# Performance work log

Measured on AMD Instinct MI355X. Metric: run time of the kernel, lower is better.

## Reference

```python
import jax, jax.numpy as jnp
import numpy as np

E = 1024   # embed_dim
H = 16     # num_heads
Dh = E // H
FF = 4 * E
LN_EPS = 1e-5


def _layernorm(x, g, b):
    mu = jnp.mean(x, axis=-1, keepdims=True)
    var = jnp.var(x, axis=-1, keepdims=True)
    return (x - mu) * jax.lax.rsqrt(var + LN_EPS) * g + b


def setup_inputs() -> dict:
    key = jax.random.key(0)
    ks = jax.random.split(key, 10)
    s = lambda fan_in: 1.0 / np.sqrt(fan_in)
    x = jax.random.normal(ks[0], (2, 2048, E), dtype=jnp.float32)
    Wq = jax.random.uniform(ks[1], (H, E, Dh), jnp.float32, -s(E), s(E))
    Wk = jax.random.uniform(ks[2], (H, E, Dh), jnp.float32, -s(E), s(E))
    Wproj = jax.random.uniform(ks[3], (E, E), jnp.float32, -s(E), s(E))
    bproj = jax.random.uniform(ks[4], (E,), jnp.float32, -s(E), s(E))
    ln1_g = jnp.ones((E,), jnp.float32)
    ln1_b = jnp.zeros((E,), jnp.float32)
    ln2_g = jnp.ones((E,), jnp.float32)
    ln2_b = jnp.zeros((E,), jnp.float32)
    W1 = jax.random.uniform(ks[5], (E, FF), jnp.float32, -s(E), s(E))
    b1 = jax.random.uniform(ks[6], (FF,), jnp.float32, -s(E), s(E))
    W2 = jax.random.uniform(ks[7], (FF, E), jnp.float32, -s(FF), s(FF))
    b2 = jax.random.uniform(ks[8], (E,), jnp.float32, -s(FF), s(FF))
    return dict(x=x, Wq=Wq, Wk=Wk, Wproj=Wproj, bproj=bproj,
                ln1_g=ln1_g, ln1_b=ln1_b, ln2_g=ln2_g, ln2_b=ln2_b,
                W1=W1, b1=b1, W2=W2, b2=b2)


def reference(x, Wq, Wk, Wproj, bproj, ln1_g, ln1_b, ln2_g, ln2_b, W1, b1, W2, b2):
    B, S, _ = x.shape
    # --- self-attention branch ---
    h = _layernorm(x, ln1_g, ln1_b)
    Q = jnp.einsum('bse,hed->bhsd', h, Wq)
    K = jnp.einsum('bse,hed->bhsd', h, Wk)
    # NOTE: original code uses V = key(x), so values == keys (faithful bug).
    scores = jnp.einsum('bhqd,bhkd->bhqk', Q, K) * (1.0 / np.sqrt(Dh))
    causal = jnp.tril(jnp.ones((S, S), dtype=bool))
    scores = jnp.where(causal, scores, -jnp.inf)
    attn = jax.nn.softmax(scores, axis=-1)  # dropout is identity in eval
    out = jnp.einsum('bhqk,bhkd->bhqd', attn, K)
    out = out.transpose(0, 2, 1, 3).reshape(B, S, H * Dh)
    x = x + out @ Wproj + bproj
    # --- MLP branch ---
    h2 = _layernorm(x, ln2_g, ln2_b)
    ff = jax.nn.relu(h2 @ W1 + b1) @ W2 + b2
    return x + ff
```

## Files before the change

### kernel.cpp

```cpp
#include <hip/hip_runtime.h>
#include <stdint.h>

typedef __bf16 bf16x8 __attribute__((ext_vector_type(8)));
typedef float f32x4 __attribute__((ext_vector_type(4)));
typedef float f32x16 __attribute__((ext_vector_type(16)));
typedef unsigned short u16;
typedef unsigned int u32;
typedef unsigned int u32x2 __attribute__((ext_vector_type(2)));

__device__ __forceinline__ u16 f2bf(float f) {
    u32 u = __builtin_bit_cast(u32, f);
    u = (u + 0x7fffu + ((u >> 16) & 1u)) >> 16;
    return (u16)u;
}
__device__ __forceinline__ float bf2f(u16 x) {
    return __builtin_bit_cast(float, (u32)x << 16);
}
__device__ __forceinline__ float fexp2(float x) {
#if __has_builtin(__builtin_amdgcn_exp2f)
    return __builtin_amdgcn_exp2f(x);
#else
    return exp2f(x);
#endif
}
__device__ __forceinline__ void plswap(u32& a, u32& b) {
#if __has_builtin(__builtin_amdgcn_permlane32_swap)
    u32x2 r = __builtin_amdgcn_permlane32_swap(a, b, false, false);
    a = r[0]; b = r[1];
#else
    asm volatile("v_permlane32_swap_b32 %0, %1" : "+v"(a), "+v"(b));
#endif
}

__device__ __forceinline__ void gload16(const u16* g, u16* l) {
    __builtin_amdgcn_global_load_lds(
        (const __attribute__((address_space(1))) unsigned int*)g,
        (__attribute__((address_space(3))) unsigned int*)l,
        16, 0, 0);
}

__device__ __constant__ unsigned char QB2[72] = {
    0,1,2,2,3,3,4,4,4,5,5,5,6,6,6,6,7,7,7,7,
    8,8,8,8,8,9,9,9,9,9,10,10,10,10,10,10,11,11,11,11,11,11,
    12,12,12,12,12,12,12,13,13,13,13,13,13,13,
    14,14,14,14,14,14,14,14,15,15,15,15,15,15,15,15};
__device__ __constant__ unsigned char CH2[72] = {
    0,0,0,1,0,1,0,1,2,0,1,2,0,1,2,3,0,1,2,3,
    0,1,2,3,4,0,1,2,3,4,0,1,2,3,4,5,0,1,2,3,4,5,
    0,1,2,3,4,5,6,0,1,2,3,4,5,6,
    0,1,2,3,4,5,6,7,0,1,2,3,4,5,6,7};
__device__ __constant__ unsigned char CUM2[17] =
    {0,1,2,4,6,9,12,16,20,25,30,36,42,49,56,64,72};

__global__ __launch_bounds__(256)
void prep_all(const float* __restrict__ Wq, const float* __restrict__ Wk,
              const float* __restrict__ Wproj, const float* __restrict__ W1,
              const float* __restrict__ W2,
              u16* __restrict__ wqkT, u16* __restrict__ wprojT,
              u16* __restrict__ w1T, u16* __restrict__ w2T,
              const float* __restrict__ x, const float* __restrict__ g1,
              const float* __restrict__ b1v, u16* __restrict__ hbuf) {
    __shared__ u16 tile[64 * 64];
    __shared__ float red[8];
    const int bid = blockIdx.x;
    const int t = threadIdx.x;
    if (bid >= 2816) {
        const int row = bid - 2816;
        float4 v = reinterpret_cast<const float4*>(x + (size_t)row * 1024)[t];
        float s = v.x + v.y + v.z + v.w;
        float sq = v.x * v.x + v.y * v.y + v.z * v.z + v.w * v.w;
        for (int o = 32; o > 0; o >>= 1) { s += __shfl_down(s, o); sq += __shfl_down(sq, o); }
        if ((t & 63) == 0) { red[t >> 6] = s; red[4 + (t >> 6)] = sq; }
        __syncthreads();
        float S  = red[0] + red[1] + red[2] + red[3];
        float SQ = red[4] + red[5] + red[6] + red[7];
        float mean = S * (1.f / 1024.f);
        float var  = SQ * (1.f / 1024.f) - mean * mean;
        float rstd = rsqrtf(var + 1e-5f);
        float4 g4 = reinterpret_cast<const float4*>(g1)[t];
        float4 b4 = reinterpret_cast<const float4*>(b1v)[t];
        ushort4 o;
        o.x = f2bf((v.x - mean) * rstd * g4.x + b4.x);
        o.y = f2bf((v.y - mean) * rstd * g4.y + b4.y);
        o.z = f2bf((v.z - mean) * rstd * g4.z + b4.z);
        o.w = f2bf((v.w - mean) * rstd * g4.w + b4.w);
        reinterpret_cast<ushort4*>(hbuf + (size_t)row * 1024)[t] = o;
        return;
    }
    const float* src; u16* dst; int R, C, c0, r0; size_t zb = 0;
    if (bid < 512) {
        const int q = bid & 255; const int z = q >> 4;
        src = (bid < 256) ? Wq : Wk;
        dst = (bid < 256) ? wqkT : (wqkT + 1048576);
        R = 1024; C = 64; c0 = 0; r0 = (q & 15) * 64; zb = (size_t)z * 65536;
    } else if (bid < 768) {
        const int q = bid - 512; src = Wproj; dst = wprojT; R = 1024; C = 1024;
        c0 = (q & 15) * 64; r0 = (q >> 4) * 64;
    } else if (bid < 1792) {
        const int q = bid - 768; src = W1; dst = w1T; R = 1024; C = 4096;
        c0 = (q & 63) * 64; r0 = (q >> 6) * 64;
    } else {
        const int q = bid - 1792; src = W2; dst = w2T; R = 4096; C = 1024;
        c0 = (q & 15) * 64; r0 = (q >> 4) * 64;
    }
    {
        const int r = t >> 2, j4 = t & 3;
        #pragma unroll
        for (int j = 0; j < 4; ++j) {
            int c = j4 * 4 + j * 16;
            float4 v = *reinterpret_cast<const float4*>(src + zb + (size_t)(r0 + r) * C + c0 + c);
            tile[(c + 0) * 64 + (r ^ (((c + 0) & 7) * 8))] = f2bf(v.x);
            tile[(c + 1) * 64 + (r ^ (((c + 1) & 7) * 8))] = f2bf(v.y);
            tile[(c + 2) * 64 + (r ^ (((c + 2) & 7) * 8))] = f2bf(v.z);
            tile[(c + 3) * 64 + (r ^ (((c + 3) & 7) * 8))] = f2bf(v.w);
        }
    }
    __syncthreads();
    {
        const int cc = t >> 2, j4 = t & 3;
        const int sw = (cc & 7) * 8;
        #pragma unroll
        for (int j2 = 0; j2 < 4; ++j2) {
            int rbase = j4 * 16 + j2 * 4;
            ushort4 o;
            o.x = tile[cc * 64 + ((rbase + 0) ^ sw)];
            o.y = tile[cc * 64 + ((rbase + 1) ^ sw)];
            o.z = tile[cc * 64 + ((rbase + 2) ^ sw)];
            o.w = tile[cc * 64 + ((rbase + 3) ^ sw)];
            *reinterpret_cast<ushort4*>(dst + zb + (size_t)(c0 + cc) * R + r0 + rbase) = o;
        }
    }
}

__global__ __launch_bounds__(256)
void ln_kernel(const float* __restrict__ x, u16* __restrict__ out,
               const float* __restrict__ gw, const float* __restrict__ bw) {
    __shared__ float red[8];
    int row = blockIdx.x, t = threadIdx.x;
    float4 v = reinterpret_cast<const float4*>(x + (size_t)row * 1024)[t];
    float s = v.x + v.y + v.z + v.w;
    float sq = v.x * v.x + v.y * v.y + v.z * v.z + v.w * v.w;
    for (int o = 32; o > 0; o >>= 1) { s += __shfl_down(s, o); sq += __shfl_down(sq, o); }
    if ((t & 63) == 0) { red[t >> 6] = s; red[4 + (t >> 6)] = sq; }
    __syncthreads();
    float S  = red[0] + red[1] + red[2] + red[3];
    float SQ = red[4] + red[5] + red[6] + red[7];
    float mean = S * (1.f / 1024.f);
    float var  = SQ * (1.f / 1024.f) - mean * mean;
    float rstd = rsqrtf(var + 1e-5f);
    float4 g4 = reinterpret_cast<const float4*>(gw)[t];
    float4 b4 = reinterpret_cast<const float4*>(bw)[t];
    ushort4 o;
    o.x = f2bf((v.x - mean) * rstd * g4.x + b4.x);
    o.y = f2bf((v.y - mean) * rstd * g4.y + b4.y);
    o.z = f2bf((v.z - mean) * rstd * g4.z + b4.z);
    o.w = f2bf((v.w - mean) * rstd * g4.w + b4.w);
    reinterpret_cast<ushort4*>(out + (size_t)row * 1024)[t] = o;
}

__global__ __launch_bounds__(256)
void ln2red_kernel(const u16* __restrict__ p0, const u16* __restrict__ p1,
                   const float4* __restrict__ x4, const float* __restrict__ bproj,
                   const float* __restrict__ gw, const float* __restrict__ bw,
                   float4* __restrict__ xmid, u16* __restrict__ out) {
    __shared__ float red[8];
    const int row = blockIdx.x, t = threadIdx.x;
    const size_t idx = (size_t)row * 256 + t;
    const ushort4 a4 = *reinterpret_cast<const ushort4*>(p0 + idx * 4);
    const ushort4 b4u = *reinterpret_cast<const ushort4*>(p1 + idx * 4);
    float4 xx = x4[idx];
    const float4 bp = *reinterpret_cast<const float4*>(bproj + (t << 2));
    float4 v;
    v.x = bf2f(a4.x) + bf2f(b4u.x) + xx.x + bp.x;
    v.y = bf2f(a4.y) + bf2f(b4u.y) + xx.y + bp.y;
    v.z = bf2f(a4.z) + bf2f(b4u.z) + xx.z + bp.z;
    v.w = bf2f(a4.w) + bf2f(b4u.w) + xx.w + bp.w;
    xmid[idx] = v;
    float s = v.x + v.y + v.z + v.w;
    float sq = v.x * v.x + v.y * v.y + v.z * v.z + v.w * v.w;
    for (int o = 32; o > 0; o >>= 1) { s += __shfl_down(s, o); sq += __shfl_down(sq, o); }
    if ((t & 63) == 0) { red[t >> 6] = s; red[4 + (t >> 6)] = sq; }
    __syncthreads();
    float S  = red[0] + red[1] + red[2] + red[3];
    float SQ = red[4] + red[5] + red[6] + red[7];
    float mean = S * (1.f / 1024.f);
    float var  = SQ * (1.f / 1024.f) - mean * mean;
    float rstd = rsqrtf(var + 1e-5f);
    const float4 g4 = *reinterpret_cast<const float4*>(gw + (t << 2));
    const float4 b4 = *reinterpret_cast<const float4*>(bw + (t << 2));
    ushort4 o;
    o.x = f2bf((v.x - mean) * rstd * g4.x + b4.x);
    o.y = f2bf((v.y - mean) * rstd * g4.y + b4.y);
    o.z = f2bf((v.z - mean) * rstd * g4.z + b4.z);
    o.w = f2bf((v.w - mean) * rstd * g4.w + b4.w);
    *reinterpret_cast<ushort4*>(out + idx * 4) = o;
}

template<int EPI, typename OT>
__global__ __launch_bounds__(256)
void gemm_bt(const u16* __restrict__ A, const u16* __restrict__ B,
             OT* __restrict__ C, const float* __restrict__ bias,
             const float* __restrict__ res, int K, int N, u16* __restrict__ ktr) {
    __shared__ u16 Al[128 * 64];
    __shared__ u16 Bl[128 * 64];
    const int t = threadIdx.x;
    const int lane = t & 63;
    const int w = t >> 6;
    const int wm = w >> 1, wn = w & 1;
    const int l15 = lane & 15, gq = lane >> 4;
    const int gx = gridDim.x;
    const int nwg = gx * gridDim.y;
    const int bid = blockIdx.y * gx + blockIdx.x;
    const int sw = ((nwg & 7) == 0) ? ((bid & 7) * (nwg >> 3) + (bid >> 3)) : bid;
    const int col0 = (sw % gx) * 128;
    const int row0 = (sw / gx) * 128;

    f32x4 acc[4][4] = {};

    const int nkb = K >> 6;
    for (int kb = 0; kb < nkb; ++kb) {
        #pragma unroll
        for (int i = 0; i < 4; ++i) {
            int slot = i * 256 + t;
            int r = slot >> 3;
            int g = (slot & 7) ^ (r & 7);
            gload16(A + (size_t)(row0 + r) * K + kb * 64 + g * 8, Al + slot * 8);
            gload16(B + (size_t)(col0 + r) * K + kb * 64 + g * 8, Bl + slot * 8);
        }
        __syncthreads();
        #pragma unroll
        for (int s = 0; s < 2; ++s) {
            bf16x8 af[4], bfr[4];
            #pragma unroll
            for (int mi = 0; mi < 4; ++mi) {
                int rl = wm * 64 + mi * 16 + l15;
                int ba = rl * 128 + ((s * 64 + gq * 16) ^ ((rl & 7) << 4));
                af[mi] = *reinterpret_cast<const bf16x8*>(reinterpret_cast<const char*>(Al) + ba);
            }
            #pragma unroll
            for (int ni = 0; ni < 4; ++ni) {
                int rl = wn * 64 + ni * 16 + l15;
                int ba = rl * 128 + ((s * 64 + gq * 16) ^ ((rl & 7) << 4));
                bfr[ni] = *reinterpret_cast<const bf16x8*>(reinterpret_cast<const char*>(Bl) + ba);
            }
            #pragma unroll
            for (int mi = 0; mi < 4; ++mi)
                #pragma unroll
                for (int ni = 0; ni < 4; ++ni)
                    acc[mi][ni] = __builtin_amdgcn_mfma_f32_16x16x32_bf16(af[mi], bfr[ni], acc[mi][ni], 0, 0, 0);
        }
        __syncthreads();
    }

    #pragma unroll
    for (int mi = 0; mi < 4; ++mi) {
        #pragma unroll
        for (int ni = 0; ni < 4; ++ni) {
            int gcol = col0 + wn * 64 + ni * 16 + l15;
            int grow0 = row0 + wm * 64 + mi * 16 + gq * 4;
            #pragma unroll
            for (int r = 0; r < 4; ++r) {
                int grow = grow0 + r;
                float v = acc[mi][ni][r];
                if constexpr (EPI == 1 || EPI == 2) v += bias[gcol];
                if constexpr (EPI == 1) v += res[(size_t)grow * N + gcol];
                if constexpr (EPI == 2) v = fmaxf(v, 0.f);
                if constexpr (sizeof(OT) == 4) C[(size_t)grow * N + gcol] = v;
                else                           C[(size_t)grow * N + gcol] = f2bf(v);
            }
        }
    }
}

#define DS_A(MH) \
  _Pragma("unroll") \
  for (int mi = 0; mi < 4; ++mi) { \
    const int rl = wm * 128 + (MH) * 64 + mi * 16 + l15; \
    const char* rp = abase + rl * 128; \
    const int sw2 = (rl & 7) << 4; \
    af[mi][0] = *reinterpret_cast<const bf16x8*>(rp + ((gq * 16) ^ sw2)); \
    af[mi][1] = *reinterpret_cast<const bf16x8*>(rp + ((64 + gq * 16) ^ sw2)); \
  }

#define DS_B(NH) \
  _Pragma("unroll") \
  for (int ni = 0; ni < 2; ++ni) { \
    const int rl = wn * 64 + (NH) * 32 + ni * 16 + l15; \
    const char* rp = bbase + rl * 128; \
    const int sw2 = (rl & 7) << 4; \
    bfr[NH][ni][0] = *reinterpret_cast<const bf16x8*>(rp + ((gq * 16) ^ sw2)); \
    bfr[NH][ni][1] = *reinterpret_cast<const bf16x8*>(rp + ((64 + gq * 16) ^ sw2)); \
  }

#define ST_A(HALF, KP, DB) \
  _Pragma("unroll") \
  for (int i = 0; i < 2; ++i) { \
    const int idx = i * 512 + t; const int rs = idx >> 3; const int kc = idx & 7; \
    const int row = (rs & 63) + ((rs >> 6) << 7) + (HALF) * 64; \
    gload16(Ag + (size_t)(row0 + row) * Kf + (KP) + ((kc ^ (row & 7)) << 3), (DB) + row * 64 + kc * 8); \
  }

#define ST_B(HALF, KP, DB) \
  _Pragma("unroll") \
  for (int i = 0; i < 2; ++i) { \
    const int idx = i * 512 + t; const int rs = idx >> 3; const int kc = idx & 7; \
    const int row = (rs & 31) + ((rs >> 5) << 6) + (HALF) * 32; \
    gload16(Bg + (size_t)(col0 + row) * Kf + (KP) + ((kc ^ (row & 7)) << 3), (DB) + row * 64 + kc * 8); \
  }

#define MFMA_Q(MH, NH) \
  _Pragma("unroll") \
  for (int mi = 0; mi < 4; ++mi) { \
    _Pragma("unroll") \
    for (int ni = 0; ni < 2; ++ni) { \
      acc[MH][mi][NH][ni] = __builtin_amdgcn_mfma_f32_16x16x32_bf16(af[mi][0], bfr[NH][ni][0], acc[MH][mi][NH][ni], 0, 0, 0); \
      acc[MH][mi][NH][ni] = __builtin_amdgcn_mfma_f32_16x16x32_bf16(af[mi][1], bfr[NH][ni][1], acc[MH][mi][NH][ni], 0, 0, 0); \
    } \
  }

#define WAITV(N) asm volatile("s_waitcnt vmcnt(" #N ")" ::: "memory")
#define BAR() __builtin_amdgcn_s_barrier()
#define PRIO1() __builtin_amdgcn_s_setprio(1)
#define PRIO0() __builtin_amdgcn_s_setprio(0)

__device__ __forceinline__ void xcd_rect(int bid, int gx, int nwg, int& colI, int& rowI) {
    if (nwg == 256 && gx == 16) {
        const int xcd = bid & 7, k = bid >> 3;
        colI = (xcd & 3) * 4 + (k & 3);
        rowI = (xcd >> 2) * 8 + (k >> 2);
    } else if (nwg == 128 && gx == 8) {
        const int xcd = bid & 7, k = bid >> 3;
        colI = (xcd & 3) * 2 + (k & 1);
        rowI = (xcd >> 2) * 8 + (k >> 1);
    } else {
        const int sw = ((nwg & 7) == 0) ? ((bid & 7) * (nwg >> 3) + (bid >> 3)) : bid;
        colI = sw % gx; rowI = sw / gx;
    }
}

template<int EPI, typename OT>
__global__ __launch_bounds__(512, 2)
void gemm256(const u16* __restrict__ A, const u16* __restrict__ B, OT* __restrict__ C,
             const float* __restrict__ bias, const float* __restrict__ res,
             int Kf, int KC, int N, u16* __restrict__ ktr) {
    __shared__ u16 AL[2][16384];
    __shared__ u16 BL[2][16384];
    const int t = threadIdx.x;
    const int lane = t & 63;
    const int w = t >> 6;
    const int wm = w >> 2, wn = w & 3;
    const int l15 = lane & 15, gq = lane >> 4;
    const int gx = gridDim.x;
    const int nwg = gx * gridDim.y;
    const int bid = blockIdx.y * gx + blockIdx.x;
    int colI, rowI;
    xcd_rect(bid, gx, nwg, colI, rowI);
    const int col0 = colI * 256;
    const int row0 = rowI * 256;
    const int kbase = blockIdx.z * KC;
    const u16* Ag = A;
    const u16* Bg = B;

    f32x4 acc[2][4][2][2] = {};
    bf16x8 af[4][2], bfr[2][2][2];

    const int NT = KC >> 6;
    { u16* An = &AL[0][0]; u16* Bn = &BL[0][0];
      ST_A(0, kbase, An); ST_B(0, kbase, Bn); ST_B(1, kbase, Bn); ST_A(1, kbase, An); }
    WAITV(4);
    BAR();

    for (int tI = 0; tI < NT - 1; ++tI) {
        const int c = tI & 1;
        const char* abase = reinterpret_cast<const char*>(&AL[c][0]);
        const char* bbase = reinterpret_cast<const char*>(&BL[c][0]);
        u16* An = &AL[c ^ 1][0];
        u16* Bn = &BL[c ^ 1][0];
        const int kn = kbase + (tI + 1) * 64;
        DS_A(0); DS_B(0);
        ST_A(0, kn, An);
        WAITV(4); BAR();
        PRIO1(); MFMA_Q(0, 0); PRIO0();
        BAR();
        DS_B(1);
        ST_B(0, kn, Bn);
        WAITV(4); BAR();
        PRIO1(); MFMA_Q(0, 1); PRIO0();
        BAR();
        DS_A(1);
        ST_B(1, kn, Bn);
        BAR();
        PRIO1(); MFMA_Q(1, 0); PRIO0();
        BAR();
        ST_A(1, kn, An);
        WAITV(4); BAR();
        PRIO1(); MFMA_Q(1, 1); PRIO0();
        BAR();
    }
    {
        const int c = (NT - 1) & 1;
        const char* abase = reinterpret_cast<const char*>(&AL[c][0]);
        const char* bbase = reinterpret_cast<const char*>(&BL[c][0]);
        DS_A(0); DS_B(0);
        WAITV(2); BAR();
        PRIO1(); MFMA_Q(0, 0); PRIO0();
        BAR();
        DS_B(1);
        WAITV(0); BAR();
        PRIO1(); MFMA_Q(0, 1); PRIO0();
        BAR();
        DS_A(1);
        BAR();
        PRIO1(); MFMA_Q(1, 0); PRIO0();
        BAR();
        PRIO1(); MFMA_Q(1, 1); PRIO0();
    }

    const size_t Crow0 = (size_t)blockIdx.z * ((size_t)gridDim.y * 256);
    #pragma unroll
    for (int mh = 0; mh < 2; ++mh)
    #pragma unroll
    for (int mi = 0; mi < 4; ++mi)
    #pragma unroll
    for (int nh = 0; nh < 2; ++nh)
    #pragma unroll
    for (int ni = 0; ni < 2; ++ni) {
        const int gcol = col0 + wn * 64 + nh * 32 + ni * 16 + l15;
        const int grow0 = row0 + wm * 128 + mh * 64 + mi * 16 + gq * 4;
        f32x4 v = acc[mh][mi][nh][ni];
        if constexpr (EPI == 2) {
            const float bb = bias[gcol];
            v[0] += bb; v[1] += bb; v[2] += bb; v[3] += bb;
        }
        #pragma unroll
        for (int r = 0; r < 4; ++r) {
            const size_t o = (Crow0 + grow0 + r) * N + gcol;
            float x = v[r];
            if constexpr (EPI == 2) x = fmaxf(x, 0.f);
            if constexpr (sizeof(OT) == 4) C[o] = x;
            else                           C[o] = f2bf(x);
        }
    }
}

#define DS_B2 \
  _Pragma("unroll") \
  for (int ni = 0; ni < 2; ++ni) { \
    const int rl = wn * 32 + ni * 16 + l15; \
    const char* rp = bbase + rl * 128; \
    const int sw2 = (rl & 7) << 4; \
    bfr[ni][0] = *reinterpret_cast<const bf16x8*>(rp + ((gq * 16) ^ sw2)); \
    bfr[ni][1] = *reinterpret_cast<const bf16x8*>(rp + ((64 + gq * 16) ^ sw2)); \
  }

#define ST_B2(KP, DB) \
  _Pragma("unroll") \
  for (int i = 0; i < 2; ++i) { \
    const int idx = i * 512 + t; const int rs = idx >> 3; const int kc = idx & 7; \
    gload16(Bg + (size_t)(col0 + rs) * Kf + (KP) + ((kc ^ (rs & 7)) << 3), (DB) + rs * 64 + kc * 8); \
  }

#define MFMA_Q2(MH) \
  _Pragma("unroll") \
  for (int mi = 0; mi < 4; ++mi) { \
    _Pragma("unroll") \
    for (int ni = 0; ni < 2; ++ni) { \
      acc[MH][mi][ni] = __builtin_amdgcn_mfma_f32_16x16x32_bf16(af[mi][0], bfr[ni][0], acc[MH][mi][ni], 0, 0, 0); \
      acc[MH][mi][ni] = __builtin_amdgcn_mfma_f32_16x16x32_bf16(af[mi][1], bfr[ni][1], acc[MH][mi][ni], 0, 0, 0); \
    } \
  }

template<int EPI, typename OT>
__global__ __launch_bounds__(512, 2)
void gemmN128(const u16* __restrict__ A, const u16* __restrict__ B, OT* __restrict__ C,
              int Kf, int KC, int N, u16* __restrict__ ktr) {
    __shared__ u16 AL[2][16384];
    __shared__ u16 BL[2][8192];
    const int t = threadIdx.x;
    const int lane = t & 63;
    const int w = t >> 6;
    const int wm = w >> 2, wn = w & 3;
    const int l15 = lane & 15, gq = lane >> 4;
    const int gx = gridDim.x;
    const int nwg = gx * gridDim.y;
    const int bid = blockIdx.y * gx + blockIdx.x;
    int colI, rowI;
    xcd_rect(bid, gx, nwg, colI, rowI);
    const int col0 = colI * 128;
    const int row0 = rowI * 256;
    const int kbase = blockIdx.z * KC;
    const u16* Ag = A;
    const u16* Bg = B;

    f32x4 acc[2][4][2] = {};
    bf16x8 af[4][2], bfr[2][2];

    const int NT = KC >> 6;
    { u16* An = &AL[0][0]; u16* Bn = &BL[0][0];
      ST_A(0, kbase, An); ST_B2(kbase, Bn); ST_A(1, kbase, An); }
    WAITV(0);
    BAR();

    for (int tI = 0; tI < NT - 1; ++tI) {
        const int c = tI & 1;
        const char* abase = reinterpret_cast<const char*>(&AL[c][0]);
        const char* bbase = reinterpret_cast<const char*>(&BL[c][0]);
        u16* An = &AL[c ^ 1][0];
        u16* Bn = &BL[c ^ 1][0];
        const int kn = kbase + (tI + 1) * 64;
        DS_A(0); DS_B2;
        ST_A(0, kn, An); ST_B2(kn, Bn);
        WAITV(4); BAR();
        PRIO1(); MFMA_Q2(0); PRIO0();
        BAR();
        DS_A(1);
        ST_A(1, kn, An);
        WAITV(2); BAR();
        PRIO1(); MFMA_Q2(1); PRIO0();
        BAR();
    }
    {
        const int c = (NT - 1) & 1;
        const char* abase = reinterpret_cast<const char*>(&AL[c][0]);
        const char* bbase = reinterpret_cast<const char*>(&BL[c][0]);
        DS_A(0); DS_B2;
        WAITV(0); BAR();
        PRIO1(); MFMA_Q2(0); PRIO0();
        BAR();
        DS_A(1);
        PRIO1(); MFMA_Q2(1); PRIO0();
    }

    const size_t Crow0 = (size_t)blockIdx.z * ((size_t)gridDim.y * 256);
    #pragma unroll
    for (int mh = 0; mh < 2; ++mh)
    #pragma unroll
    for (int mi = 0; mi < 4; ++mi)
    #pragma unroll
    for (int ni = 0; ni < 2; ++ni) {
        const int gcol = col0 + wn * 32 + ni * 16 + l15;
        const int grow0 = row0 + wm * 128 + mh * 64 + mi * 16 + gq * 4;
        f32x4 v = acc[mh][mi][ni];
        if constexpr (EPI == 3) {
            if (gcol < 1024) {
                const float QS = 0.18033688f;
                v[0] *= QS; v[1] *= QS; v[2] *= QS; v[3] *= QS;
            }
        }
        #pragma unroll
        for (int r = 0; r < 4; ++r) {
            const size_t o = (Crow0 + grow0 + r) * N + gcol;
            if constexpr (sizeof(OT) == 4) C[o] = v[r];
            else                           C[o] = f2bf(v[r]);
        }
        if constexpr (EPI == 3) {
            if (gcol >= 1024) {
                ushort4 k4;
                k4.x = f2bf(v[0]); k4.y = f2bf(v[1]); k4.z = f2bf(v[2]); k4.w = f2bf(v[3]);
                *reinterpret_cast<ushort4*>(ktr + (size_t)(gcol - 1024) * 4096 + grow0) = k4;
            }
        }
    }
}

__global__ __launch_bounds__(256)
void reduce2_kernel(const u16* __restrict__ p0, const u16* __restrict__ p1,
                    const float4* __restrict__ xm, const float* __restrict__ b2,
                    float4* __restrict__ out) {
    const size_t i = (size_t)blockIdx.x * 256 + threadIdx.x;
    const ushort4 a4 = *reinterpret_cast<const ushort4*>(p0 + i * 4);
    const ushort4 b4 = *reinterpret_cast<const ushort4*>(p1 + i * 4);
    float4 x = xm[i];
    const float4 bb = *reinterpret_cast<const float4*>(b2 + ((threadIdx.x & 255) << 2));
    float4 o;
    o.x = x.x + bb.x + bf2f(a4.x) + bf2f(b4.x);
    o.y = x.y + bb.y + bf2f(a4.y) + bf2f(b4.y);
    o.z = x.z + bb.z + bf2f(a4.z) + bf2f(b4.z);
    o.w = x.w + bb.w + bf2f(a4.w) + bf2f(b4.w);
    out[i] = o;
}

template<int SPLIT>
__global__ __launch_bounds__(256)
void attn_kernel(const u16* __restrict__ qk, const u16* __restrict__ ktr, u16* __restrict__ out,
                 u16* __restrict__ pO, float* __restrict__ pl) {
    __shared__ u16 Kl[2][64 * 64];
    __shared__ u16 Tl[2][64 * 64];
    const int t = threadIdx.x;
    const int lane = t & 63;
    const int w = t >> 6;
    const int l31 = lane & 31, hi = lane >> 5;
    int bh, qb, npc, cid, s0, s1;
    if constexpr (SPLIT) {
        bh = blockIdx.x & 31;
        cid = blockIdx.x >> 5;
        qb = QB2[cid];
        const int ch = CH2[cid];
        npc = CUM2[qb + 1] - CUM2[qb];
        const int nt = 2 * (qb + 1);
        s0 = ch * 4;
        s1 = min(nt, s0 + 4);
    } else {
        bh = blockIdx.x & 31;
        const int tt = blockIdx.x >> 5;
        qb = (tt < 8) ? tt : 23 - tt;
        cid = 0; npc = 1; s0 = 0; s1 = 2 * (qb + 1);
    }
    const int b = bh >> 4, h = bh & 15;
    const int q0w = qb * 128 + w * 32;
    const int q = q0w + l31;
    const int qwmax = q0w + 31;
    const u16* Qp = qk + (size_t)b * 2048 * 2048 + h * 64;
    const u16* Kp = Qp + 1024;
    const u16* Tp = ktr + (size_t)h * 64 * 4096 + (size_t)b * 2048;

    bf16x8 qf[4];
    #pragma unroll
    for (int s = 0; s < 4; ++s)
        qf[s] = *reinterpret_cast<const bf16x8*>(Qp + (size_t)q * 2048 + s * 16 + hi * 8);

    f32x16 oacc[2] = {};
    float lsum = 0.f;

    {
        #pragma unroll
        for (int i = 0; i < 2; ++i) {
            int slot = i * 256 + t;
            int r = slot >> 3;
            int g = (slot & 7) ^ (r & 7);
            gload16(Kp + (size_t)(s0 * 64 + r) * 2048 + g * 8, &Kl[0][0] + slot * 8);
            gload16(Tp + (size_t)r * 4096 + s0 * 64 + g * 8, &Tl[0][0] + slot * 8);
        }
    }

    for (int kt = s0; kt < s1; ++kt) {
        const int cur = (kt - s0) & 1;
        __syncthreads();
        if (kt + 1 < s1) {
            int k0 = (kt + 1) * 64;
            #pragma unroll
            for (int i = 0; i < 2; ++i) {
                int slot = i * 256 + t;
                int r = slot >> 3;
                int g = (slot & 7) ^ (r & 7);
                gload16(Kp + (size_t)(k0 + r) * 2048 + g * 8, &Kl[cur ^ 1][0] + slot * 8);
                gload16(Tp + (size_t)r * 4096 + k0 + g * 8, &Tl[cur ^ 1][0] + slot * 8);
            }
        }
        const int kbase = kt * 64;
        if (kbase > qwmax) continue;
        const u16* kl = &Kl[cur][0];
        const u16* tl = &Tl[cur][0];

        f32x16 st0 = {}, st1 = {};
        PRIO1();
        #pragma unroll
        for (int s = 0; s < 4; ++s) {
            {
                int r = l31;
                int col = (16 * s + 8 * hi) ^ ((r & 7) * 8);
                bf16x8 kf = *reinterpret_cast<const bf16x8*>(kl + r * 64 + col);
                st0 = __builtin_amdgcn_mfma_f32_32x32x16_bf16(kf, qf[s], st0, 0, 0, 0);
            }
            {
                int r = 32 + l31;
                int col = (16 * s + 8 * hi) ^ ((r & 7) * 8);
                bf16x8 kf = *reinterpret_cast<const bf16x8*>(kl + r * 64 + col);
                st1 = __builtin_amdgcn_mfma_f32_32x32x16_bf16(kf, qf[s], st1, 0, 0, 0);
            }
        }
        PRIO0();

        float p[32];
        if (kbase + 63 <= q0w) {
            #pragma unroll
            for (int i = 0; i < 16; ++i) { p[i] = st0[i]; p[16 + i] = st1[i]; }
        } else {
            #pragma unroll
            for (int i = 0; i < 16; ++i) {
                int kloc = kbase + (i & 3) + 8 * (i >> 2) + 4 * hi;
                p[i]      = (kloc      <= q) ? st0[i] : -3.0e38f;
                p[16 + i] = (kloc + 32 <= q) ? st1[i] : -3.0e38f;
            }
        }
        #pragma unroll
        for (int i = 0; i < 32; ++i) p[i] = fexp2(p[i]);
        float s0v = 0.f, s1v = 0.f, s2v = 0.f, s3v = 0.f;
        #pragma unroll
        for (int i = 0; i < 8; ++i) {
            s0v += p[4 * i]; s1v += p[4 * i + 1]; s2v += p[4 * i + 2]; s3v += p[4 * i + 3];
        }
        lsum += (s0v + s1v) + (s2v + s3v);

        u32 wds[16];
        #pragma unroll
        for (int j = 0; j < 16; ++j) {
            u16 a = __builtin_bit_cast(u16, (__bf16)p[2 * j]);
            u16 c = __builtin_bit_cast(u16, (__bf16)p[2 * j + 1]);
            wds[j] = (u32)a | ((u32)c << 16);
        }
        union PF { u32 wd[4]; bf16x8 b; } pf[4];
        #pragma unroll
        for (int qd = 0; qd < 4; ++qd) {
            u32 a = wds[4 * qd + 0], bb = wds[4 * qd + 2];
            u32 c = wds[4 * qd + 1], d = wds[4 * qd + 3];
            plswap(a, bb);
            plswap(c, d);
            pf[qd].wd[0] = a; pf[qd].wd[1] = c; pf[qd].wd[2] = bb; pf[qd].wd[3] = d;
        }
        PRIO1();
        #pragma unroll
        for (int kc = 0; kc < 4; ++kc) {
            #pragma unroll
            for (int db = 0; db < 2; ++db) {
                int r = db * 32 + l31;
                int col = (kc * 16 + 8 * hi) ^ ((r & 7) * 8);
                bf16x8 vf = *reinterpret_cast<const bf16x8*>(tl + r * 64 + col);
                oacc[db] = __builtin_amdgcn_mfma_f32_32x32x16_bf16(vf, pf[kc].b, oacc[db], 0, 0, 0);
            }
        }
        PRIO0();
    }

    lsum += __shfl_xor(lsum, 32);

    if (npc == 1) {
        const float inv = 1.f / lsum;
        u16* op = out + (size_t)(b * 2048 + q) * 1024 + h * 64;
        #pragma unroll
        for (int db = 0; db < 2; ++db) {
            #pragma unroll
            for (int tq = 0; tq < 4; ++tq) {
                ushort4 o;
                o.x = f2bf(oacc[db][tq * 4 + 0] * inv);
                o.y = f2bf(oacc[db][tq * 4 + 1] * inv);
                o.z = f2bf(oacc[db][tq * 4 + 2] * inv);
                o.w = f2bf(oacc[db][tq * 4 + 3] * inv);
                *reinterpret_cast<ushort4*>(op + db * 32 + tq * 8 + hi * 4) = o;
            }
        }
    } else {
        const size_t g = (size_t)bh * 72 + cid;
        u16* po = pO + (g * 128 + (w * 32 + l31)) * 64;
        #pragma unroll
        for (int db = 0; db < 2; ++db) {
            #pragma unroll
            for (int tq = 0; tq < 4; ++tq) {
                ushort4 o;
                o.x = f2bf(oacc[db][tq * 4 + 0]);
                o.y = f2bf(oacc[db][tq * 4 + 1]);
                o.z = f2bf(oacc[db][tq * 4 + 2]);
                o.w = f2bf(oacc[db][tq * 4 + 3]);
                *reinterpret_cast<ushort4*>(po + db * 32 + tq * 8 + hi * 4) = o;
            }
        }
        if (hi == 0)
            pl[g * 128 + w * 32 + l31] = lsum;
    }
}

__global__ __launch_bounds__(256)
void attn_combine(const u16* __restrict__ pO, const float* __restrict__ pl,
                  u16* __restrict__ out) {
    const int g = blockIdx.x;
    const int bh = g & 31;
    const int qb = 2 + (g >> 5);
    const int b = bh >> 4, h = bh & 15;
    const int base = bh * 72 + CUM2[qb];
    const int npc = CUM2[qb + 1] - CUM2[qb];
    const int t = threadIdx.x;
    const int q = t >> 1;
    const int dh = (t & 1) << 5;

    float L = 0.f;
    float o[32] = {};
    for (int p = 0; p < 8; ++p) {
        if (p >= npc) break;
        L += pl[(size_t)(base + p) * 128 + q];
        const u16* src = pO + ((size_t)(base + p) * 128 + q) * 64 + dh;
        #pragma unroll
        for (int j = 0; j < 8; ++j) {
            ushort4 v = *reinterpret_cast<const ushort4*>(src + j * 4);
            o[4 * j + 0] += bf2f(v.x);
            o[4 * j + 1] += bf2f(v.y);
            o[4 * j + 2] += bf2f(v.z);
            o[4 * j + 3] += bf2f(v.w);
        }
    }
    const float inv = 1.f / L;
    u16* dst = out + ((size_t)(b * 2048 + qb * 128 + q)) * 1024 + h * 64 + dh;
    #pragma unroll
    for (int j = 0; j < 8; ++j) {
        ushort4 w4;
        w4.x = f2bf(o[4 * j + 0] * inv);
        w4.y = f2bf(o[4 * j + 1] * inv);
        w4.z = f2bf(o[4 * j + 2] * inv);
        w4.w = f2bf(o[4 * j + 3] * inv);
        *reinterpret_cast<ushort4*>(dst + j * 4) = w4;
    }
}

extern "C" void kernel_launch(void* const* d_in, const int* in_sizes, int n_in,
                              void* d_out, int out_size, void* d_ws, size_t ws_size,
                              hipStream_t stream) {
    const float* x     = (const float*)d_in[0];
    const float* Wq    = (const float*)d_in[1];
    const float* Wk    = (const float*)d_in[2];
    const float* Wproj = (const float*)d_in[3];
    const float* bproj = (const float*)d_in[4];
    const float* ln1g  = (const float*)d_in[5];
    const float* ln1b  = (const float*)d_in[6];
    const float* ln2g  = (const float*)d_in[7];
    const float* ln2b  = (const float*)d_in[8];
    const float* W1    = (const float*)d_in[9];
    const float* b1    = (const float*)d_in[10];
    const float* W2    = (const float*)d_in[11];
    const float* b2    = (const float*)d_in[12];

    char* ws = (char*)d_ws;
    u16*   wqkT   = (u16*)(ws + 0);
    u16*   wprojT = (u16*)(ws + (4ull << 20));
    u16*   w1T    = (u16*)(ws + (6ull << 20));
    u16*   w2T    = (u16*)(ws + (14ull << 20));
    u16*   hbuf   = (u16*)(ws + (22ull << 20));
    float* xmid   = (float*)(ws + (30ull << 20));
    u16*   qk     = (u16*)(ws + (46ull << 20));
    u16*   ktr    = (u16*)(ws + (62ull << 20));
    u16*   attnb  = (u16*)(ws + (70ull << 20));
    u16*   ff     = (u16*)(ws + (46ull << 20));
    u16*   pO16   = (u16*)(ws + (78ull << 20));
    u16*   pg     = (u16*)(ws + (78ull << 20));
    float* pl     = (float*)(ws + (118ull << 20));
    const bool fast = ws_size >= (142ull << 20);

    prep_all<<<6912, 256, 0, stream>>>(Wq, Wk, Wproj, W1, W2,
                                       wqkT, wprojT, w1T, w2T,
                                       x, ln1g, ln1b, hbuf);
    gemmN128<3, u16><<<dim3(16, 16, 1), 512, 0, stream>>>(hbuf, wqkT, qk, 1024, 1024, 2048, ktr);
    if (fast) {
        attn_kernel<1><<<2304, 256, 0, stream>>>(qk, ktr, attnb, pO16, pl);
        attn_combine<<<448, 256, 0, stream>>>(pO16, pl, attnb);
    } else {
        attn_kernel<0><<<512, 256, 0, stream>>>(qk, ktr, attnb, nullptr, nullptr);
    }
    if (fast) {
        gemmN128<0, u16><<<dim3(8, 16, 2), 512, 0, stream>>>(attnb, wprojT, pg, 1024, 512, 1024, nullptr);
        ln2red_kernel<<<4096, 256, 0, stream>>>(
            pg, pg + 4194304, (const float4*)x,
            bproj, ln2g, ln2b, (float4*)xmid, hbuf);
    } else {
        gemm_bt<1, float><<<dim3(8, 32), 256, 0, stream>>>(attnb, wprojT, xmid, bproj, x, 1024, 1024, nullptr);
        ln_kernel<<<4096, 256, 0, stream>>>(xmid, hbuf, ln2g, ln2b);
    }
    gemm256<2, u16><<<dim3(16, 16, 1), 512, 0, stream>>>(hbuf, w1T, ff, b1, nullptr, 1024, 1024, 4096, nullptr);
    if (fast) {
        gemmN128<0, u16><<<dim3(8, 16, 2), 512, 0, stream>>>(ff, w2T, pg, 4096, 2048, 1024, nullptr);
        reduce2_kernel<<<4096, 256, 0, stream>>>(
            pg, pg + 4194304, (const float4*)xmid, b2, (float4*)d_out);
    } else {
        gemm_bt<1, float><<<dim3(8, 32), 256, 0, stream>>>(ff, w2T, (float*)d_out, b2, xmid, 4096, 1024, nullptr);
    }
}
```

Baseline: 209.7 us.

## Load attention K/V tiles directly from global memory instead of LDS staging

Removes the double-buffered shared-memory staging of K and transposed-K tiles in the attention kernel. Each wave now reads its MFMA operands straight from global memory (relying on L1/L2 caches), which drops the __syncthreads barriers and lets waves exit early with break once past the causal diagonal. The cost is redundant global/cache traffic, since all four waves now fetch the same K tiles, and the loads lose their explicit prefetch overlap, so memory latency is exposed.

```diff
diff --git a/kernel.cpp b/kernel.cpp
--- a/kernel.cpp
+++ b/kernel.cpp
@@ -584,8 +584,6 @@
 __global__ __launch_bounds__(256)
 void attn_kernel(const u16* __restrict__ qk, const u16* __restrict__ ktr, u16* __restrict__ out,
                  u16* __restrict__ pO, float* __restrict__ pl) {
-    __shared__ u16 Kl[2][64 * 64];
-    __shared__ u16 Tl[2][64 * 64];
     const int t = threadIdx.x;
     const int lane = t & 63;
     const int w = t >> 6;
@@ -622,52 +620,20 @@
     f32x16 oacc[2] = {};
     float lsum = 0.f;
 
-    {
-        #pragma unroll
-        for (int i = 0; i < 2; ++i) {
-            int slot = i * 256 + t;
-            int r = slot >> 3;
-            int g = (slot & 7) ^ (r & 7);
-            gload16(Kp + (size_t)(s0 * 64 + r) * 2048 + g * 8, &Kl[0][0] + slot * 8);
-            gload16(Tp + (size_t)r * 4096 + s0 * 64 + g * 8, &Tl[0][0] + slot * 8);
-        }
-    }
-
     for (int kt = s0; kt < s1; ++kt) {
-        const int cur = (kt - s0) & 1;
-        __syncthreads();
-        if (kt + 1 < s1) {
-            int k0 = (kt + 1) * 64;
-            #pragma unroll
-            for (int i = 0; i < 2; ++i) {
-                int slot = i * 256 + t;
-                int r = slot >> 3;
-                int g = (slot & 7) ^ (r & 7);
-                gload16(Kp + (size_t)(k0 + r) * 2048 + g * 8, &Kl[cur ^ 1][0] + slot * 8);
-                gload16(Tp + (size_t)r * 4096 + k0 + g * 8, &Tl[cur ^ 1][0] + slot * 8);
-            }
-        }
         const int kbase = kt * 64;
-        if (kbase > qwmax) continue;
-        const u16* kl = &Kl[cur][0];
-        const u16* tl = &Tl[cur][0];
+        if (kbase > qwmax) break;
 
         f32x16 st0 = {}, st1 = {};
         PRIO1();
         #pragma unroll
         for (int s = 0; s < 4; ++s) {
-            {
-                int r = l31;
-                int col = (16 * s + 8 * hi) ^ ((r & 7) * 8);
-                bf16x8 kf = *reinterpret_cast<const bf16x8*>(kl + r * 64 + col);
-                st0 = __builtin_amdgcn_mfma_f32_32x32x16_bf16(kf, qf[s], st0, 0, 0, 0);
-            }
-            {
-                int r = 32 + l31;
-                int col = (16 * s + 8 * hi) ^ ((r & 7) * 8);
-                bf16x8 kf = *reinterpret_cast<const bf16x8*>(kl + r * 64 + col);
-                st1 = __builtin_amdgcn_mfma_f32_32x32x16_bf16(kf, qf[s], st1, 0, 0, 0);
-            }
+            bf16x8 kf0 = *reinterpret_cast<const bf16x8*>(
+                Kp + (size_t)(kbase + l31) * 2048 + s * 16 + hi * 8);
+            st0 = __builtin_amdgcn_mfma_f32_32x32x16_bf16(kf0, qf[s], st0, 0, 0, 0);
+            bf16x8 kf1 = *reinterpret_cast<const bf16x8*>(
+                Kp + (size_t)(kbase + 32 + l31) * 2048 + s * 16 + hi * 8);
+            st1 = __builtin_amdgcn_mfma_f32_32x32x16_bf16(kf1, qf[s], st1, 0, 0, 0);
         }
         PRIO0();
 
@@ -713,9 +679,8 @@
         for (int kc = 0; kc < 4; ++kc) {
             #pragma unroll
             for (int db = 0; db < 2; ++db) {
-                int r = db * 32 + l31;
-                int col = (kc * 16 + 8 * hi) ^ ((r & 7) * 8);
-                bf16x8 vf = *reinterpret_cast<const bf16x8*>(tl + r * 64 + col);
+                bf16x8 vf = *reinterpret_cast<const bf16x8*>(
+                    Tp + (size_t)(db * 32 + l31) * 4096 + kbase + kc * 16 + hi * 8);
                 oacc[db] = __builtin_amdgcn_mfma_f32_32x32x16_bf16(vf, pf[kc].b, oacc[db], 0, 0, 0);
             }
         }
```

New measurement: 245.5 us. 17.1% more time.
